# Optimization experiments

Hardware: AMD Instinct MI355X
Metric: run time of the kernel (lower is better)

Reference implementation:

```python
import jax, jax.numpy as jnp
import numpy as np

N_HEAD = 16

def setup_inputs() -> dict:
    key = jax.random.key(0)
    ks = jax.random.split(key, 5)
    B, T, C = 4, 2048, 1024
    s = 0.02
    return {
        "x": jax.random.normal(ks[0], (B, T, C), dtype=jnp.float32),
        "W_attn": jax.random.normal(ks[1], (C, 3 * C), dtype=jnp.float32) * s,
        "b_attn": jax.random.normal(ks[2], (3 * C,), dtype=jnp.float32) * s,
        "W_proj": jax.random.normal(ks[3], (C, C), dtype=jnp.float32) * s,
        "b_proj": jax.random.normal(ks[4], (C,), dtype=jnp.float32) * s,
    }

def reference(x, W_attn, b_attn, W_proj, b_proj):
    B, T, C = x.shape
    H = N_HEAD
    D = C // H
    qkv = x @ W_attn + b_attn                      # [B,T,3C]
    q, k, v = jnp.split(qkv, 3, axis=2)
    # [B,H,T,D]
    q = q.reshape(B, T, H, D).transpose(0, 2, 1, 3)
    k = k.reshape(B, T, H, D).transpose(0, 2, 1, 3)
    v = v.reshape(B, T, H, D).transpose(0, 2, 1, 3)
    scale = 1.0 / jnp.sqrt(jnp.float32(D))
    att = jnp.einsum('bhqd,bhkd->bhqk', q, k) * scale
    causal = jnp.tril(jnp.ones((T, T), dtype=bool))
    att = jnp.where(causal[None, None], att, -jnp.inf)
    att = jax.nn.softmax(att, axis=-1)
    y = jnp.einsum('bhqk,bhkd->bhqd', att, v)       # [B,H,T,D]
    y = y.transpose(0, 2, 1, 3).reshape(B, T, C)
    return y @ W_proj + b_proj
```

## Files before the change

### kernel.cpp

```cpp
#include <hip/hip_runtime.h>

typedef unsigned short u16;
typedef unsigned int u32;
typedef __bf16 bf16x8 __attribute__((ext_vector_type(8)));
typedef short s16x4 __attribute__((ext_vector_type(4)));
typedef float f32x4 __attribute__((ext_vector_type(4)));

#define MFMA16(a,b,c) __builtin_amdgcn_mfma_f32_16x16x32_bf16((a),(b),(c),0,0,0)

#if defined(__has_builtin)
#if __has_builtin(__builtin_amdgcn_mfma_f32_16x16x16bf16_1k)
#define MFMA1K(a,b,c) __builtin_amdgcn_mfma_f32_16x16x16bf16_1k((a),(b),(c),0,0,0)
#endif
#endif
#ifndef MFMA1K
__device__ __forceinline__ f32x4 mfma1k_asm(s16x4 a, s16x4 b, f32x4 c) {
    f32x4 d;
    asm volatile("v_mfma_f32_16x16x16_bf16 %0, %1, %2, %3"
                 : "=v"(d) : "v"(a), "v"(b), "0"(c));
    return d;
}
#define MFMA1K(a,b,c) mfma1k_asm((a),(b),(c))
#endif

__device__ __forceinline__ float b2f(u16 u) {
    u32 v = ((u32)u) << 16;
    return __builtin_bit_cast(float, v);
}
__device__ __forceinline__ u16 f2b(float f) {
    u32 u = __builtin_bit_cast(u32, f);
    u = u + 0x7FFFu + ((u >> 16) & 1u);
    return (u16)(u >> 16);
}

__device__ __forceinline__ void gload_lds16(const u16* g, u16* l) {
    __builtin_amdgcn_global_load_lds(
        (__attribute__((address_space(1))) void*)g,
        (__attribute__((address_space(3))) void*)l, 16, 0, 0);
}

__device__ __forceinline__ uint4 load8_bf16(const void* base, size_t off, int f32m) {
    if (f32m) {
        const float* p = (const float*)base + off;
        float4 a = *(const float4*)p;
        float4 b = *(const float4*)(p + 4);
        union { u16 u[8]; uint4 v; } t;
        t.u[0] = f2b(a.x); t.u[1] = f2b(a.y); t.u[2] = f2b(a.z); t.u[3] = f2b(a.w);
        t.u[4] = f2b(b.x); t.u[5] = f2b(b.y); t.u[6] = f2b(b.z); t.u[7] = f2b(b.w);
        return t.v;
    }
    return *(const uint4*)((const u16*)base + off);
}

__global__ __launch_bounds__(256) void k_detect(const u16* __restrict__ x, int* flag) {
    __shared__ int c;
    if (threadIdx.x == 0) c = 0;
    __syncthreads();
    int my = 0;
    #pragma unroll
    for (int j = 0; j < 16; ++j) {
        u16 v = x[2 * (threadIdx.x + 256 * j)];
        if (((v >> 7) & 0xFF) >= 0x90) ++my;
    }
    atomicAdd(&c, my);
    __syncthreads();
    if (threadIdx.x == 0) *flag = (c > 64) ? 1 : 0;
}

__global__ __launch_bounds__(256) void k_cvt_bias(
    const void* __restrict__ ba, const void* __restrict__ bp,
    const int* __restrict__ flag, u16* __restrict__ bac, u16* __restrict__ bpc)
{
    const int f32m = *flag;
    const int t = threadIdx.x;
    #pragma unroll
    for (int j = 0; j < 12; ++j) {
        int i = t + 256 * j;
        if (i < 3072) bac[i] = f32m ? f2b(((const float*)ba)[i]) : ((const u16*)ba)[i];
    }
    #pragma unroll
    for (int j = 0; j < 4; ++j) {
        int i = t + 256 * j;
        if (i < 1024) bpc[i] = f32m ? f2b(((const float*)bp)[i]) : ((const u16*)bp)[i];
    }
}

__global__ __launch_bounds__(256) void k_cvt_x(
    const float* __restrict__ x, const int* __restrict__ flag, u16* __restrict__ out)
{
    if (!*flag) return;
    size_t i = ((size_t)blockIdx.x * 256 + threadIdx.x) * 8;
    float4 a = *(const float4*)(x + i);
    float4 b = *(const float4*)(x + i + 4);
    union { u16 u[8]; uint4 v; } t;
    t.u[0] = f2b(a.x); t.u[1] = f2b(a.y); t.u[2] = f2b(a.z); t.u[3] = f2b(a.w);
    t.u[4] = f2b(b.x); t.u[5] = f2b(b.y); t.u[6] = f2b(b.z); t.u[7] = f2b(b.w);
    *(uint4*)(out + i) = t.v;
}

__global__ __launch_bounds__(256) void k_transpose(
    const void* __restrict__ src, u16* __restrict__ dst, int R, int Cc,
    const int* __restrict__ flag)
{
    __shared__ u16 tile[64 * 72];
    const int f32m = *flag;
    const int t = threadIdx.x;
    const int c0 = blockIdx.x * 64, r0 = blockIdx.y * 64;
    #pragma unroll
    for (int i = 0; i < 2; ++i) {
        int ch = t + 256 * i;
        int r = ch >> 3, c8 = (ch & 7) * 8;
        *(uint4*)&tile[r * 72 + c8] =
            load8_bf16(src, (size_t)(r0 + r) * Cc + c0 + c8, f32m);
    }
    __syncthreads();
    #pragma unroll
    for (int i = 0; i < 2; ++i) {
        int ch = t + 256 * i;
        int r = ch >> 3, c8 = (ch & 7) * 8;
        union { u16 u[8]; uint4 v; } tmp;
        #pragma unroll
        for (int j = 0; j < 8; ++j) tmp.u[j] = tile[(c8 + j) * 72 + r];
        *(uint4*)&dst[(size_t)(c0 + r) * R + r0 + c8] = tmp.v;
    }
}

__global__ __launch_bounds__(256) void k_gemm_qkv(
    const void* __restrict__ x, const u16* __restrict__ Abf,
    const u16* __restrict__ Bt, const u16* __restrict__ bias,
    const int* __restrict__ flag,
    u16* __restrict__ Ql, u16* __restrict__ Kl, u16* __restrict__ Vt)
{
    constexpr int K = 1024;
    __shared__ __align__(16) u16 As[128 * 64];
    __shared__ __align__(16) u16 Bs[128 * 64];
    const int t = threadIdx.x;
    const int lane = t & 63, w = t >> 6;
    const int quad = lane >> 4, m16 = lane & 15;
    const int wm = (w >> 1) * 64, wn = (w & 1) * 64;
    const int m0 = blockIdx.x * 128, n0 = blockIdx.y * 128;
    const int lr = lane >> 3;
    const int lc = (lane & 7) * 8;
    const u16* A = (*flag) ? Abf : (const u16*)x;

    const f32x4 z = {0.f, 0.f, 0.f, 0.f};
    f32x4 acc[4][4];
    #pragma unroll
    for (int mi = 0; mi < 4; ++mi)
        #pragma unroll
        for (int ni = 0; ni < 4; ++ni) acc[mi][ni] = z;

    for (int k0 = 0; k0 < K; k0 += 64) {
        __syncthreads();
        #pragma unroll
        for (int i = 0; i < 4; ++i) {
            const int chunk = w * 4 + i;
            const int row = chunk * 8 + lr;
            gload_lds16(&A [(size_t)(m0 + row) * K + k0 + lc], &As[chunk * 512]);
            gload_lds16(&Bt[(size_t)(n0 + row) * K + k0 + lc], &Bs[chunk * 512]);
        }
        __syncthreads();
        #pragma unroll
        for (int kk = 0; kk < 2; ++kk) {
            bf16x8 af[4], bfr[4];
            #pragma unroll
            for (int mi = 0; mi < 4; ++mi)
                af[mi] = *(const bf16x8*)&As[(wm + mi * 16 + m16) * 64 + kk * 32 + quad * 8];
            #pragma unroll
            for (int ni = 0; ni < 4; ++ni)
                bfr[ni] = *(const bf16x8*)&Bs[(wn + ni * 16 + m16) * 64 + kk * 32 + quad * 8];
            #pragma unroll
            for (int mi = 0; mi < 4; ++mi)
                #pragma unroll
                for (int ni = 0; ni < 4; ++ni)
                    acc[mi][ni] = MFMA16(af[mi], bfr[ni], acc[mi][ni]);
        }
    }

    const int sec = n0 >> 10;
    const float qscale = (sec == 0) ? 0.18033688011112042f : 1.0f;
    #pragma unroll
    for (int mi = 0; mi < 4; ++mi) {
        #pragma unroll
        for (int ni = 0; ni < 4; ++ni) {
            int gn = n0 + wn + ni * 16 + m16;
            int sn = gn & 1023;
            int h = sn >> 6, d = sn & 63;
            float bv = b2f(bias[gn]);
            #pragma unroll
            for (int v = 0; v < 4; ++v) {
                int gm = m0 + wm + mi * 16 + quad * 4 + v;
                int bb = gm >> 11, tt = gm & 2047;
                u16 o = f2b((acc[mi][ni][v] + bv) * qscale);
                size_t bh = (size_t)(bb * 16 + h);
                if (sec == 0)      Ql[(bh * 2048 + tt) * 64 + d] = o;
                else if (sec == 1) Kl[(bh * 2048 + tt) * 64 + d] = o;
                else               Vt[(bh * 64 + d) * 2048 + tt] = o;
            }
        }
    }
}

__global__ __launch_bounds__(256) void k_attn(
    u16* __restrict__ Ql, const u16* __restrict__ Kl, const u16* __restrict__ Vt)
{
    __shared__ u16 Ks[128 * 80];
    __shared__ u16 Vs[64 * 136];
    const int t = threadIdx.x;
    const int lane = t & 63, w = t >> 6;
    const int quad = lane >> 4, m16 = lane & 15;
    const int qb = 15 - (blockIdx.x >> 6);
    const int bh = blockIdx.x & 63;
    const int q0 = qb * 128;

    bf16x8 fq[2][2];
    #pragma unroll
    for (int s = 0; s < 2; ++s) {
        const u16* Qp = Ql + ((size_t)bh * 2048 + q0 + s * 64 + w * 16 + m16) * 64;
        fq[s][0] = *(const bf16x8*)&Qp[quad * 8];
        fq[s][1] = *(const bf16x8*)&Qp[32 + quad * 8];
    }

    const f32x4 z = {0.f, 0.f, 0.f, 0.f};
    f32x4 acco[2][4] = {{z, z, z, z}, {z, z, z, z}};
    float lsum[2] = {0.f, 0.f};

    const int ktmax = qb;
    const u16* Kbase = Kl + (size_t)bh * 2048 * 64;
    const u16* Vbase = Vt + (size_t)bh * 64 * 2048;

    uint4 kreg[4], vreg[4];
    #pragma unroll
    for (int i = 0; i < 4; ++i) {
        int c = t + 256 * i;
        int r = c >> 3, col = (c & 7) * 8;
        kreg[i] = *(const uint4*)&Kbase[(size_t)r * 64 + col];
        int dd = c >> 4, kvc = (c & 15) * 8;
        vreg[i] = *(const uint4*)&Vbase[(size_t)dd * 2048 + kvc];
    }

    for (int kt = 0; kt <= ktmax; ++kt) {
        __syncthreads();
        #pragma unroll
        for (int i = 0; i < 4; ++i) {
            int c = t + 256 * i;
            int r = c >> 3, col = (c & 7) * 8;
            *(uint4*)&Ks[r * 80 + col] = kreg[i];
            int dd = c >> 4, kvc = (c & 15) * 8;
            *(uint4*)&Vs[dd * 136 + kvc] = vreg[i];
        }
        __syncthreads();

        if (kt < ktmax) {
            #pragma unroll
            for (int i = 0; i < 4; ++i) {
                int c = t + 256 * i;
                int r = c >> 3, col = (c & 7) * 8;
                kreg[i] = *(const uint4*)&Kbase[(size_t)((kt + 1) * 128 + r) * 64 + col];
                int dd = c >> 4, kvc = (c & 15) * 8;
                vreg[i] = *(const uint4*)&Vbase[(size_t)dd * 2048 + (kt + 1) * 128 + kvc];
            }
        }

        const bool diag = (kt == ktmax);
        #pragma unroll
        for (int s = 0; s < 2; ++s) {
            f32x4 accs[8] = {z, z, z, z, z, z, z, z};
            #pragma unroll
            for (int kk = 0; kk < 2; ++kk)
                #pragma unroll
                for (int ni = 0; ni < 8; ++ni) {
                    bf16x8 bk = *(const bf16x8*)&Ks[(ni * 16 + m16) * 80 + kk * 32 + quad * 8];
                    accs[ni] = MFMA16(bk, fq[s][kk], accs[ni]);
                }

            const int qg = q0 + s * 64 + w * 16 + m16;
            s16x4 pkv[8];
            #pragma unroll
            for (int ni = 0; ni < 8; ++ni) {
                union { __bf16 b[4]; s16x4 sv; } pk;
                #pragma unroll
                for (int v = 0; v < 4; ++v) {
                    float sc = accs[ni][v];
                    if (diag && (kt * 128 + ni * 16 + quad * 4 + v > qg)) sc = -30000.0f;
                    float pe = __builtin_amdgcn_exp2f(sc);
                    pk.b[v] = (__bf16)pe;
                    lsum[s] += pe;
                }
                pkv[ni] = pk.sv;
            }

            #pragma unroll
            for (int ni = 0; ni < 8; ++ni) {
                #pragma unroll
                for (int nd = 0; nd < 4; ++nd) {
                    s16x4 va = *(const s16x4*)&Vs[(nd * 16 + m16) * 136 + ni * 16 + quad * 4];
                    acco[s][nd] = MFMA1K(va, pkv[ni], acco[s][nd]);
                }
            }
        }
    }

    #pragma unroll
    for (int s = 0; s < 2; ++s) {
        lsum[s] += __shfl_xor(lsum[s], 16);
        lsum[s] += __shfl_xor(lsum[s], 32);
    }

    #pragma unroll
    for (int s = 0; s < 2; ++s) {
        const int qg = q0 + s * 64 + w * 16 + m16;
        const float inv = 1.0f / fmaxf(lsum[s], 1e-30f);
        u16* Orow = &Ql[((size_t)bh * 2048 + qg) * 64];
        #pragma unroll
        for (int nd = 0; nd < 4; ++nd) {
            union { u16 u[4]; uint2 uu; } o;
            #pragma unroll
            for (int v = 0; v < 4; ++v) o.u[v] = f2b(acco[s][nd][v] * inv);
            *(uint2*)&Orow[nd * 16 + quad * 4] = o.uu;
        }
    }
}

__global__ __launch_bounds__(256) void k_gemm_proj(
    const u16* __restrict__ Yl, const u16* __restrict__ Bt, const u16* __restrict__ bias,
    const int* __restrict__ flag, void* __restrict__ Out)
{
    constexpr int K = 1024;
    __shared__ __align__(16) u16 As[128 * 64];
    __shared__ __align__(16) u16 Bs[128 * 64];
    const int f32m = *flag;
    const int t = threadIdx.x;
    const int lane = t & 63, w = t >> 6;
    const int quad = lane >> 4, m16 = lane & 15;
    const int wm = (w >> 1) * 64, wn = (w & 1) * 64;
    const int m0 = blockIdx.x * 128, n0 = blockIdx.y * 128;
    const int bb = m0 >> 11, t0 = m0 & 2047;
    const int lr = lane >> 3;
    const int lc = (lane & 7) * 8;

    const f32x4 z = {0.f, 0.f, 0.f, 0.f};
    f32x4 acc[4][4];
    #pragma unroll
    for (int mi = 0; mi < 4; ++mi)
        #pragma unroll
        for (int ni = 0; ni < 4; ++ni) acc[mi][ni] = z;

    for (int k0 = 0; k0 < K; k0 += 64) {
        const int h = k0 >> 6;
        const u16* Abase = Yl + ((size_t)(bb * 16 + h) * 2048 + t0) * 64;
        __syncthreads();
        #pragma unroll
        for (int i = 0; i < 4; ++i) {
            const int chunk = w * 4 + i;
            gload_lds16(&Abase[chunk * 512 + lane * 8], &As[chunk * 512]);
            gload_lds16(&Bt[(size_t)(n0 + chunk * 8 + lr) * K + k0 + lc], &Bs[chunk * 512]);
        }
        __syncthreads();
        #pragma unroll
        for (int kk = 0; kk < 2; ++kk) {
            bf16x8 af[4], bfr[4];
            #pragma unroll
            for (int mi = 0; mi < 4; ++mi)
                af[mi] = *(const bf16x8*)&As[(wm + mi * 16 + m16) * 64 + kk * 32 + quad * 8];
            #pragma unroll
            for (int ni = 0; ni < 4; ++ni)
                bfr[ni] = *(const bf16x8*)&Bs[(wn + ni * 16 + m16) * 64 + kk * 32 + quad * 8];
            #pragma unroll
            for (int mi = 0; mi < 4; ++mi)
                #pragma unroll
                for (int ni = 0; ni < 4; ++ni)
                    acc[mi][ni] = MFMA16(af[mi], bfr[ni], acc[mi][ni]);
        }
    }

    #pragma unroll
    for (int mi = 0; mi < 4; ++mi) {
        #pragma unroll
        for (int ni = 0; ni < 4; ++ni) {
            int gn = n0 + wn + ni * 16 + m16;
            float bv = b2f(bias[gn]);
            #pragma unroll
            for (int v = 0; v < 4; ++v) {
                int gm = m0 + wm + mi * 16 + quad * 4 + v;
                float val = acc[mi][ni][v] + bv;
                if (f32m) ((float*)Out)[(size_t)gm * 1024 + gn] = val;
                else      ((u16*)Out)[(size_t)gm * 1024 + gn] = f2b(val);
            }
        }
    }
}

extern "C" void kernel_launch(void* const* d_in, const int* in_sizes, int n_in,
                              void* d_out, int out_size, void* d_ws, size_t ws_size,
                              hipStream_t stream)
{
    (void)in_sizes; (void)n_in; (void)out_size; (void)ws_size;
    const void* x  = d_in[0];
    const void* Wa = d_in[1];
    const void* ba = d_in[2];
    const void* Wp = d_in[3];
    const void* bp = d_in[4];
    char* ws = (char*)d_ws;

    u16* Ql  = (u16*)(ws + 0);
    u16* Kl  = (u16*)(ws + 16777216);
    u16* Vt  = (u16*)(ws + 33554432);
    u16* WpT = (u16*)(ws + 50331648);
    int* flag = (int*)(ws + 52428800);
    u16* bpc  = (u16*)(ws + 52428800 + 256);
    u16* bac  = (u16*)(ws + 52428800 + 256 + 2048);
    u16* WaT = (u16*)d_out;
    u16* Abf = (u16*)((char*)d_out + 6291456);

    k_detect<<<1, 256, 0, stream>>>((const u16*)x, flag);
    k_cvt_bias<<<1, 256, 0, stream>>>(ba, bp, flag, bac, bpc);
    k_cvt_x<<<4096, 256, 0, stream>>>((const float*)x, flag, Abf);
    k_transpose<<<dim3(48, 16), 256, 0, stream>>>(Wa, WaT, 1024, 3072, flag);
    k_transpose<<<dim3(16, 16), 256, 0, stream>>>(Wp, WpT, 1024, 1024, flag);
    k_gemm_qkv<<<dim3(64, 24), 256, 0, stream>>>(x, Abf, WaT, bac, flag, Ql, Kl, Vt);
    k_attn<<<1024, 256, 0, stream>>>(Ql, Kl, Vt);
    k_gemm_proj<<<dim3(64, 8), 256, 0, stream>>>(Ql, WpT, bpc, flag, d_out);
}
```

Before: 336.9 us.

## Fuse prep kernels, store V row-major with LDS transpose, split diagonal mask path

Merges the detect, bias conversion, x conversion and both weight transposes into one prep kernel. Each block recomputes the dtype detection with a ballot over a sparser sample, which removes five launches and their serialization. The QKV GEMM now writes V in the same row-major layout as K, which avoids the strided transposed stores. The attention kernel then transposes V into shared memory through scalar LDS writes with a new padding. Masking is also split into a separate diagonal-only branch, so off-diagonal tiles skip the compare, at the cost of possible LDS bank conflicts in the V transpose.

New measurement: 297.3 us. -11.7%, faster.

```diff
diff --git a/kernel.cpp b/kernel.cpp
--- a/kernel.cpp
+++ b/kernel.cpp
@@ -52,60 +52,24 @@
     return *(const uint4*)((const u16*)base + off);
 }
 
-__global__ __launch_bounds__(256) void k_detect(const u16* __restrict__ x, int* flag) {
-    __shared__ int c;
-    if (threadIdx.x == 0) c = 0;
+__device__ __forceinline__ int detect_f32(const u16* __restrict__ x) {
+    __shared__ int cnt;
+    if (threadIdx.x == 0) cnt = 0;
     __syncthreads();
-    int my = 0;
-    #pragma unroll
-    for (int j = 0; j < 16; ++j) {
-        u16 v = x[2 * (threadIdx.x + 256 * j)];
-        if (((v >> 7) & 0xFF) >= 0x90) ++my;
-    }
-    atomicAdd(&c, my);
+    int my = ((x[2 * (threadIdx.x * 128)] >> 7) & 0xFF) >= 0x90;
+    unsigned long long b = __ballot(my);
+    if ((threadIdx.x & 63) == 0) atomicAdd(&cnt, (int)__popcll(b));
     __syncthreads();
-    if (threadIdx.x == 0) *flag = (c > 64) ? 1 : 0;
-}
-
-__global__ __launch_bounds__(256) void k_cvt_bias(
-    const void* __restrict__ ba, const void* __restrict__ bp,
-    const int* __restrict__ flag, u16* __restrict__ bac, u16* __restrict__ bpc)
-{
-    const int f32m = *flag;
+    return cnt > 32;
+}
+
+__device__ __forceinline__ void transpose_tile(
+    const void* __restrict__ src, u16* __restrict__ dst, int R, int Cc,
+    int f32m, int bx, int by)
+{
+    __shared__ u16 tile[64 * 72];
     const int t = threadIdx.x;
-    #pragma unroll
-    for (int j = 0; j < 12; ++j) {
-        int i = t + 256 * j;
-        if (i < 3072) bac[i] = f32m ? f2b(((const float*)ba)[i]) : ((const u16*)ba)[i];
-    }
-    #pragma unroll
-    for (int j = 0; j < 4; ++j) {
-        int i = t + 256 * j;
-        if (i < 1024) bpc[i] = f32m ? f2b(((const float*)bp)[i]) : ((const u16*)bp)[i];
-    }
-}
-
-__global__ __launch_bounds__(256) void k_cvt_x(
-    const float* __restrict__ x, const int* __restrict__ flag, u16* __restrict__ out)
-{
-    if (!*flag) return;
-    size_t i = ((size_t)blockIdx.x * 256 + threadIdx.x) * 8;
-    float4 a = *(const float4*)(x + i);
-    float4 b = *(const float4*)(x + i + 4);
-    union { u16 u[8]; uint4 v; } t;
-    t.u[0] = f2b(a.x); t.u[1] = f2b(a.y); t.u[2] = f2b(a.z); t.u[3] = f2b(a.w);
-    t.u[4] = f2b(b.x); t.u[5] = f2b(b.y); t.u[6] = f2b(b.z); t.u[7] = f2b(b.w);
-    *(uint4*)(out + i) = t.v;
-}
-
-__global__ __launch_bounds__(256) void k_transpose(
-    const void* __restrict__ src, u16* __restrict__ dst, int R, int Cc,
-    const int* __restrict__ flag)
-{
-    __shared__ u16 tile[64 * 72];
-    const int f32m = *flag;
-    const int t = threadIdx.x;
-    const int c0 = blockIdx.x * 64, r0 = blockIdx.y * 64;
+    const int c0 = bx * 64, r0 = by * 64;
     #pragma unroll
     for (int i = 0; i < 2; ++i) {
         int ch = t + 256 * i;
@@ -125,11 +89,56 @@
     }
 }
 
+__global__ __launch_bounds__(256) void k_prep(
+    const u16* __restrict__ x, const void* __restrict__ Wa,
+    const void* __restrict__ ba, const void* __restrict__ Wp,
+    const void* __restrict__ bp,
+    u16* __restrict__ WaT, u16* __restrict__ WpT, u16* __restrict__ Abf,
+    u16* __restrict__ bac, u16* __restrict__ bpc, int* __restrict__ flag)
+{
+    const int f32m = detect_f32(x);
+    int task = blockIdx.x;
+    if (task < 768) {
+        transpose_tile(Wa, WaT, 1024, 3072, f32m, task % 48, task / 48);
+        return;
+    }
+    task -= 768;
+    if (task < 256) {
+        transpose_tile(Wp, WpT, 1024, 1024, f32m, task % 16, task / 16);
+        return;
+    }
+    task -= 256;
+    if (task < 4096) {
+        if (!f32m) return;
+        size_t i = ((size_t)task * 256 + threadIdx.x) * 8;
+        const float* xf = (const float*)x;
+        float4 a = *(const float4*)(xf + i);
+        float4 b = *(const float4*)(xf + i + 4);
+        union { u16 u[8]; uint4 v; } t;
+        t.u[0] = f2b(a.x); t.u[1] = f2b(a.y); t.u[2] = f2b(a.z); t.u[3] = f2b(a.w);
+        t.u[4] = f2b(b.x); t.u[5] = f2b(b.y); t.u[6] = f2b(b.z); t.u[7] = f2b(b.w);
+        *(uint4*)(Abf + i) = t.v;
+        return;
+    }
+    const int t = threadIdx.x;
+    #pragma unroll
+    for (int j = 0; j < 12; ++j) {
+        int i = t + 256 * j;
+        if (i < 3072) bac[i] = f32m ? f2b(((const float*)ba)[i]) : ((const u16*)ba)[i];
+    }
+    #pragma unroll
+    for (int j = 0; j < 4; ++j) {
+        int i = t + 256 * j;
+        if (i < 1024) bpc[i] = f32m ? f2b(((const float*)bp)[i]) : ((const u16*)bp)[i];
+    }
+    if (t == 0) *flag = f32m;
+}
+
 __global__ __launch_bounds__(256) void k_gemm_qkv(
     const void* __restrict__ x, const u16* __restrict__ Abf,
     const u16* __restrict__ Bt, const u16* __restrict__ bias,
     const int* __restrict__ flag,
-    u16* __restrict__ Ql, u16* __restrict__ Kl, u16* __restrict__ Vt)
+    u16* __restrict__ Ql, u16* __restrict__ Kl, u16* __restrict__ Vl)
 {
     constexpr int K = 1024;
     __shared__ __align__(16) u16 As[128 * 64];
@@ -179,6 +188,7 @@
 
     const int sec = n0 >> 10;
     const float qscale = (sec == 0) ? 0.18033688011112042f : 1.0f;
+    u16* Outp = (sec == 0) ? Ql : (sec == 1) ? Kl : Vl;
     #pragma unroll
     for (int mi = 0; mi < 4; ++mi) {
         #pragma unroll
@@ -193,19 +203,17 @@
                 int bb = gm >> 11, tt = gm & 2047;
                 u16 o = f2b((acc[mi][ni][v] + bv) * qscale);
                 size_t bh = (size_t)(bb * 16 + h);
-                if (sec == 0)      Ql[(bh * 2048 + tt) * 64 + d] = o;
-                else if (sec == 1) Kl[(bh * 2048 + tt) * 64 + d] = o;
-                else               Vt[(bh * 64 + d) * 2048 + tt] = o;
+                Outp[(bh * 2048 + tt) * 64 + d] = o;
             }
         }
     }
 }
 
 __global__ __launch_bounds__(256) void k_attn(
-    u16* __restrict__ Ql, const u16* __restrict__ Kl, const u16* __restrict__ Vt)
+    u16* __restrict__ Ql, const u16* __restrict__ Kl, const u16* __restrict__ Vl)
 {
     __shared__ u16 Ks[128 * 80];
-    __shared__ u16 Vs[64 * 136];
+    __shared__ u16 Vs[64 * 132];
     const int t = threadIdx.x;
     const int lane = t & 63, w = t >> 6;
     const int quad = lane >> 4, m16 = lane & 15;
@@ -227,7 +235,7 @@
 
     const int ktmax = qb;
     const u16* Kbase = Kl + (size_t)bh * 2048 * 64;
-    const u16* Vbase = Vt + (size_t)bh * 64 * 2048;
+    const u16* Vbase = Vl + (size_t)bh * 2048 * 64;
 
     uint4 kreg[4], vreg[4];
     #pragma unroll
@@ -235,8 +243,7 @@
         int c = t + 256 * i;
         int r = c >> 3, col = (c & 7) * 8;
         kreg[i] = *(const uint4*)&Kbase[(size_t)r * 64 + col];
-        int dd = c >> 4, kvc = (c & 15) * 8;
-        vreg[i] = *(const uint4*)&Vbase[(size_t)dd * 2048 + kvc];
+        vreg[i] = *(const uint4*)&Vbase[(size_t)r * 64 + col];
     }
 
     for (int kt = 0; kt <= ktmax; ++kt) {
@@ -246,8 +253,10 @@
             int c = t + 256 * i;
             int r = c >> 3, col = (c & 7) * 8;
             *(uint4*)&Ks[r * 80 + col] = kreg[i];
-            int dd = c >> 4, kvc = (c & 15) * 8;
-            *(uint4*)&Vs[dd * 136 + kvc] = vreg[i];
+            union { u16 u[8]; uint4 v; } tv; tv.v = vreg[i];
+            #pragma unroll
+            for (int j = 0; j < 8; ++j)
+                Vs[(col + j) * 132 + r] = tv.u[j];
         }
         __syncthreads();
 
@@ -257,8 +266,7 @@
                 int c = t + 256 * i;
                 int r = c >> 3, col = (c & 7) * 8;
                 kreg[i] = *(const uint4*)&Kbase[(size_t)((kt + 1) * 128 + r) * 64 + col];
-                int dd = c >> 4, kvc = (c & 15) * 8;
-                vreg[i] = *(const uint4*)&Vbase[(size_t)dd * 2048 + (kt + 1) * 128 + kvc];
+                vreg[i] = *(const uint4*)&Vbase[(size_t)((kt + 1) * 128 + r) * 64 + col];
             }
         }
 
@@ -274,27 +282,41 @@
                     accs[ni] = MFMA16(bk, fq[s][kk], accs[ni]);
                 }
 
-            const int qg = q0 + s * 64 + w * 16 + m16;
             s16x4 pkv[8];
+            if (!diag) {
+                #pragma unroll
+                for (int ni = 0; ni < 8; ++ni) {
+                    union { __bf16 b[4]; s16x4 sv; } pk;
+                    #pragma unroll
+                    for (int v = 0; v < 4; ++v) {
+                        float pe = __builtin_amdgcn_exp2f(accs[ni][v]);
+                        pk.b[v] = (__bf16)pe;
+                        lsum[s] += pe;
+                    }
+                    pkv[ni] = pk.sv;
+                }
+            } else {
+                const int qg = q0 + s * 64 + w * 16 + m16;
+                #pragma unroll
+                for (int ni = 0; ni < 8; ++ni) {
+                    union { __bf16 b[4]; s16x4 sv; } pk;
+                    #pragma unroll
+                    for (int v = 0; v < 4; ++v) {
+                        float sc = accs[ni][v];
+                        if (kt * 128 + ni * 16 + quad * 4 + v > qg) sc = -30000.0f;
+                        float pe = __builtin_amdgcn_exp2f(sc);
+                        pk.b[v] = (__bf16)pe;
+                        lsum[s] += pe;
+                    }
+                    pkv[ni] = pk.sv;
+                }
+            }
+
             #pragma unroll
             for (int ni = 0; ni < 8; ++ni) {
-                union { __bf16 b[4]; s16x4 sv; } pk;
-                #pragma unroll
-                for (int v = 0; v < 4; ++v) {
-                    float sc = accs[ni][v];
-                    if (diag && (kt * 128 + ni * 16 + quad * 4 + v > qg)) sc = -30000.0f;
-                    float pe = __builtin_amdgcn_exp2f(sc);
-                    pk.b[v] = (__bf16)pe;
-                    lsum[s] += pe;
-                }
-                pkv[ni] = pk.sv;
-            }
-
-            #pragma unroll
-            for (int ni = 0; ni < 8; ++ni) {
                 #pragma unroll
                 for (int nd = 0; nd < 4; ++nd) {
-                    s16x4 va = *(const s16x4*)&Vs[(nd * 16 + m16) * 136 + ni * 16 + quad * 4];
+                    s16x4 va = *(const s16x4*)&Vs[(nd * 16 + m16) * 132 + ni * 16 + quad * 4];
                     acco[s][nd] = MFMA1K(va, pkv[ni], acco[s][nd]);
                 }
             }
@@ -405,7 +427,7 @@
 
     u16* Ql  = (u16*)(ws + 0);
     u16* Kl  = (u16*)(ws + 16777216);
-    u16* Vt  = (u16*)(ws + 33554432);
+    u16* Vl  = (u16*)(ws + 33554432);
     u16* WpT = (u16*)(ws + 50331648);
     int* flag = (int*)(ws + 52428800);
     u16* bpc  = (u16*)(ws + 52428800 + 256);
@@ -413,12 +435,9 @@
     u16* WaT = (u16*)d_out;
     u16* Abf = (u16*)((char*)d_out + 6291456);
 
-    k_detect<<<1, 256, 0, stream>>>((const u16*)x, flag);
-    k_cvt_bias<<<1, 256, 0, stream>>>(ba, bp, flag, bac, bpc);
-    k_cvt_x<<<4096, 256, 0, stream>>>((const float*)x, flag, Abf);
-    k_transpose<<<dim3(48, 16), 256, 0, stream>>>(Wa, WaT, 1024, 3072, flag);
-    k_transpose<<<dim3(16, 16), 256, 0, stream>>>(Wp, WpT, 1024, 1024, flag);
-    k_gemm_qkv<<<dim3(64, 24), 256, 0, stream>>>(x, Abf, WaT, bac, flag, Ql, Kl, Vt);
-    k_attn<<<1024, 256, 0, stream>>>(Ql, Kl, Vt);
+    k_prep<<<5121, 256, 0, stream>>>((const u16*)x, Wa, ba, Wp, bp,
+                                     WaT, WpT, Abf, bac, bpc, flag);
+    k_gemm_qkv<<<dim3(64, 24), 256, 0, stream>>>(x, Abf, WaT, bac, flag, Ql, Kl, Vl);
+    k_attn<<<1024, 256, 0, stream>>>(Ql, Kl, Vl);
     k_gemm_proj<<<dim3(64, 8), 256, 0, stream>>>(Ql, WpT, bpc, flag, d_out);
 }
```
